# Kernel tuning notes

Measured on AMD Instinct MI355X. Metric: run time of the kernel, lower is better.

Reference implementation:

```python
import jax, jax.numpy as jnp
import numpy as np

B, Q, D = 8, 128, 2048
H, HD = 16, 128           # num_heads, head_dim (D == H*HD)
CACHE = 3968              # tokens already in KV cache; CACHE+Q == max_seq_len


def setup_inputs() -> dict:
    key = jax.random.key(0)
    ks = jax.random.split(key, 6)
    x = jax.random.normal(ks[0], (B, Q, D), dtype=jnp.float32)
    k_cache = jax.random.normal(ks[1], (B, H, CACHE, HD), dtype=jnp.float32)
    v_cache = jax.random.normal(ks[2], (B, H, CACHE, HD), dtype=jnp.float32)
    Wqkv = jax.random.normal(ks[3], (D, 3 * D), dtype=jnp.float32) * 0.02
    Wproj = jax.random.normal(ks[4], (D, D), dtype=jnp.float32) * 0.02
    bproj = jnp.zeros((D,), dtype=jnp.float32)
    return {"x": x, "k_cache": k_cache, "v_cache": v_cache,
            "Wqkv": Wqkv, "Wproj": Wproj, "bproj": bproj}


def reference(x, k_cache, v_cache, Wqkv, Wproj, bproj):
    # QKV projection (qkv_bias=False)
    qkv = x @ Wqkv                                   # [B, Q, 3D]
    qkv = qkv.reshape(B, Q, 3, H, HD)
    qkv = jnp.transpose(qkv, (2, 0, 3, 1, 4))        # [3, B, H, Q, HD]
    q, k_new, v_new = qkv[0], qkv[1], qkv[2]
    # KV-cache append (cache_pos + Q == max_seq_len, no roll)
    k_all = jnp.concatenate([k_cache, k_new], axis=2)  # [B, H, K, HD]
    v_all = jnp.concatenate([v_cache, v_new], axis=2)
    K = CACHE + Q
    scale = 1.0 / jnp.sqrt(jnp.float32(HD))
    scores = jnp.einsum('bhqd,bhkd->bhqk', q, k_all) * scale  # [B, H, Q, K]
    # Causal mask aligned to cache (bottom-right): query i sees keys j <= i + (K - Q)
    i = jnp.arange(Q)[:, None]
    j = jnp.arange(K)[None, :]
    mask = j > (i + (K - Q))
    scores = jnp.where(mask, jnp.float32(-jnp.inf), scores)
    attn = jax.nn.softmax(scores, axis=-1)
    out = jnp.einsum('bhqk,bhkd->bhqd', attn, v_all)   # [B, H, Q, HD]
    out = jnp.transpose(out, (0, 2, 1, 3)).reshape(B, Q, D)
    return out @ Wproj + bproj
```

## Files before the change

### kernel.cpp

```cpp
#include <hip/hip_runtime.h>

typedef unsigned int u32;
typedef unsigned short u16;
typedef short s16x8 __attribute__((ext_vector_type(8)));
typedef float f32x4 __attribute__((ext_vector_type(4)));

#define MFMA16(a,b,c) __builtin_amdgcn_mfma_f32_16x16x32_bf16((a),(b),(c),0,0,0)

#define Bb 8
#define Hh 16
#define Qq 128
#define HDd 128
#define Dd 2048
#define CACHE 3968
#define NSPLIT 8
#define SCALE 0.08838834764831845f
#define SM_OFF 8.0f

__device__ __forceinline__ u16 f2bf(float x){
  u32 u = __builtin_bit_cast(u32, x);
  u32 r = ((u >> 16) & 1u) + 0x7fffu;
  return (u16)((u + r) >> 16);
}
__device__ __forceinline__ float bf2f(u16 h){
  return __builtin_bit_cast(float, ((u32)h) << 16);
}
__device__ __forceinline__ u32 pk2(float a, float b){
  return (u32)f2bf(a) | ((u32)f2bf(b) << 16);
}
__device__ __forceinline__ float f4c(const float4& v, int j){
  return j==0 ? v.x : j==1 ? v.y : j==2 ? v.z : v.w;
}
__device__ __forceinline__ void gload_lds16(const void* g, void* l){
  __builtin_amdgcn_global_load_lds(
      (const __attribute__((address_space(1))) u32*)g,
      (__attribute__((address_space(3))) u32*)l, 16, 0, 0);
}
__device__ __forceinline__ void lgkm_barrier(){
  asm volatile("s_waitcnt lgkmcnt(0)" ::: "memory");
  __builtin_amdgcn_s_barrier();
}

__global__ void k_cvt(const float* __restrict__ s, u16* __restrict__ d, int n4){
  int i = blockIdx.x * 256 + threadIdx.x;
  if (i < n4){
    float4 v = *(const float4*)(s + (size_t)i * 4);
    *(uint2*)(d + (size_t)i * 4) = make_uint2(pk2(v.x, v.y), pk2(v.z, v.w));
  }
}

__global__ void k_tcvt(const float* __restrict__ s, u16* __restrict__ d, int R, int C){
  __shared__ float t[32][33];
  int tx = threadIdx.x & 31, ty = threadIdx.x >> 5;
  int c0 = blockIdx.x * 32, r0 = blockIdx.y * 32;
#pragma unroll
  for (int i = 0; i < 4; i++)
    t[ty + i*8][tx] = s[(size_t)(r0 + ty + i*8) * C + c0 + tx];
  __syncthreads();
#pragma unroll
  for (int i = 0; i < 4; i++)
    d[(size_t)(c0 + ty + i*8) * R + r0 + tx] = f2bf(t[tx][ty + i*8]);
}

template<int MODE>
__global__ __launch_bounds__(256)
void k_gemm(const u16* __restrict__ A, const u16* __restrict__ Bt, int K, int N,
            u16* __restrict__ oq, u16* __restrict__ ok, u16* __restrict__ ov,
            float* __restrict__ of, const float* __restrict__ bias)
{
  const int m0 = blockIdx.y * 128, n0 = blockIdx.x * 128;
  const int tid = threadIdx.x;
  const int w = tid >> 6, l = tid & 63;
  const int lg = l >> 4, lr = l & 15;
  const int wr = w >> 1, wc = w & 1;

  __shared__ u16 As[2][128 * 32];
  __shared__ u16 Bs[2][128 * 32];

  f32x4 acc[4][4];
#pragma unroll
  for (int i = 0; i < 4; i++)
#pragma unroll
    for (int j = 0; j < 4; j++) acc[i][j] = f32x4{0.f, 0.f, 0.f, 0.f};

  const int nt = K >> 5;

  auto stage = [&](int buf, int t){
    const int k0 = t << 5;
#pragma unroll
    for (int i = 0; i < 2; i++){
      int flat = i * 256 + tid;
      int row = flat >> 2, kq = flat & 3;
      const u16* ga = A + (size_t)(m0 + row) * K + k0 + kq * 8;
      gload_lds16(ga, (char*)&As[buf][0] + (size_t)(i*256 + w*64) * 16);
      const u16* gb = Bt + (size_t)(n0 + row) * K + k0 + kq * 8;
      gload_lds16(gb, (char*)&Bs[buf][0] + (size_t)(i*256 + w*64) * 16);
    }
  };

  stage(0, 0);
  asm volatile("s_waitcnt vmcnt(0)" ::: "memory");
  __syncthreads();

  for (int t = 0; t < nt; ++t){
    const int buf = t & 1;
    if (t + 1 < nt) stage(buf ^ 1, t + 1);
    s16x8 af[4], bfr[4];
#pragma unroll
    for (int i = 0; i < 4; i++){
      int row = wr*64 + i*16 + lr;
      af[i] = *(const s16x8*)&As[buf][row*32 + lg*8];
    }
#pragma unroll
    for (int j = 0; j < 4; j++){
      int col = wc*64 + j*16 + lr;
      bfr[j] = *(const s16x8*)&Bs[buf][col*32 + lg*8];
    }
#pragma unroll
    for (int i = 0; i < 4; i++)
#pragma unroll
      for (int j = 0; j < 4; j++)
        acc[i][j] = MFMA16(af[i], bfr[j], acc[i][j]);
    asm volatile("s_waitcnt vmcnt(0)" ::: "memory");
    __syncthreads();
  }

#pragma unroll
  for (int i = 0; i < 4; i++){
#pragma unroll
    for (int j = 0; j < 4; j++){
#pragma unroll
      for (int r = 0; r < 4; r++){
        int m = m0 + wr*64 + i*16 + lg*4 + r;
        int n = n0 + wc*64 + j*16 + lr;
        float v = acc[i][j][r];
        if (MODE == 0){
          int which = n >> 11;
          int h = (n >> 7) & 15, hd = n & 127;
          int b = m >> 7, qi = m & 127;
          size_t idx = (((size_t)(b * Hh + h)) * Qq + qi) * HDd + hd;
          if (which == 0)      oq[idx] = f2bf(v * SCALE);
          else if (which == 1) ok[idx] = f2bf(v);
          else                 ov[idx] = f2bf(v);
        } else {
          of[(size_t)m * N + n] = v + bias[n];
        }
      }
    }
  }
}

__global__ __launch_bounds__(512, 2)
void k_attn(const float* __restrict__ kc, const float* __restrict__ vc,
            const u16* __restrict__ qw, const u16* __restrict__ knw,
            const u16* __restrict__ vnw, float* __restrict__ opart,
            float2* __restrict__ ml)
{
  const int tid = threadIdx.x;
  const int w = tid >> 6, l = tid & 63;
  const int lg = l >> 4, lr = l & 15;

  __shared__ __align__(16) u16 Ks[2][64 * 136];
  __shared__ u32 Vts[128 * 32];

  const int rv = tid & 15, c4v = tid >> 4;

#pragma unroll 1
  for (int rep = 0; rep < 2; ++rep){
    const int vb = blockIdx.x * 2 + rep;
    const int bh = vb >> 3;
    const int sg = vb & 7;

    s16x8 qf[4];
    {
      const u16* qp = qw + (((size_t)bh * Qq + w*16 + lr) * HDd);
#pragma unroll
      for (int kk = 0; kk < 4; kk++) qf[kk] = *(const s16x8*)(qp + kk*32 + lg*8);
    }

    f32x4 acc[8];
#pragma unroll
    for (int i = 0; i < 8; i++) acc[i] = f32x4{0.f, 0.f, 0.f, 0.f};
    float lpart = 0.f;

    const float* kbase = kc + (size_t)bh * CACHE * HDd;
    const float* vbase = vc + (size_t)bh * CACHE * HDd;
    const u16* knb = knw + (size_t)bh * Qq * HDd;
    const u16* vnb = vnw + (size_t)bh * Qq * HDd;

    float4 kreg[4], vreg[4];

    auto loadc = [&](int c){
      if (c < 62){
#pragma unroll
        for (int i = 0; i < 4; i++){
          int flat = tid + i*512;
          int row = flat >> 5, c4 = flat & 31;
          kreg[i] = *(const float4*)(kbase + ((size_t)(c*64 + row)) * HDd + c4*4);
        }
#pragma unroll
        for (int a = 0; a < 4; a++)
          vreg[a] = *(const float4*)(vbase + ((size_t)(c*64 + rv + a*16)) * HDd + c4v*4);
      } else {
#pragma unroll
        for (int i = 0; i < 4; i++){
          int flat = tid + i*512;
          int row = flat >> 5, c4 = flat & 31;
          ushort4 u = *(const ushort4*)(knb + ((size_t)(c*64 + row - CACHE)) * HDd + c4*4);
          kreg[i] = make_float4(bf2f(u.x), bf2f(u.y), bf2f(u.z), bf2f(u.w));
        }
#pragma unroll
        for (int a = 0; a < 4; a++){
          ushort4 u = *(const ushort4*)(vnb + ((size_t)(c*64 + rv + a*16 - CACHE)) * HDd + c4v*4);
          vreg[a] = make_float4(bf2f(u.x), bf2f(u.y), bf2f(u.z), bf2f(u.w));
        }
      }
    };

    auto writeK = [&](int buf){
#pragma unroll
      for (int i = 0; i < 4; i++){
        int flat = tid + i*512;
        int row = flat >> 5, c4 = flat & 31;
        *(uint2*)&Ks[buf][row*136 + c4*4] =
            make_uint2(pk2(kreg[i].x, kreg[i].y), pk2(kreg[i].z, kreg[i].w));
      }
    };
    auto writeV = [&](){
#pragma unroll
      for (int j = 0; j < 4; j++){
        int col = c4v*4 + j;
        int x2 = (col & 7) << 2;
        Vts[col*32 + (rv ^ x2)]        = pk2(f4c(vreg[0], j), f4c(vreg[1], j));
        Vts[col*32 + ((rv + 16) ^ x2)] = pk2(f4c(vreg[2], j), f4c(vreg[3], j));
      }
    };

    int cur = 0;
    loadc(sg * 8);
    writeK(0);
    writeV();
    __syncthreads();

    for (int cl = 0; cl < 8; ++cl){
      const int c = sg * 8 + cl;
      if (cl + 1 < 8) loadc(c + 1);

      f32x4 s[4];
      __builtin_amdgcn_s_setprio(1);
#pragma unroll
      for (int t = 0; t < 4; t++){
        s[t] = f32x4{0.f, 0.f, 0.f, 0.f};
        const u16* kp = &Ks[cur][(t*16 + lr) * 136];
#pragma unroll
        for (int kk = 0; kk < 4; kk++){
          s16x8 kf = *(const s16x8*)(kp + kk*32 + lg*8);
          s[t] = MFMA16(kf, qf[kk], s[t]);
        }
      }
      __builtin_amdgcn_s_setprio(0);

      if (c >= 62){
        int jn = c*64 - CACHE;
        int qi = w*16 + lr;
#pragma unroll
        for (int t = 0; t < 4; t++)
#pragma unroll
          for (int r = 0; r < 4; r++){
            int kn = jn + t*16 + lg*4 + r;
            if (kn > qi) s[t][r] = -__builtin_inff();
          }
      }

      float ps = 0.f;
#pragma unroll
      for (int t = 0; t < 4; t++)
#pragma unroll
        for (int r = 0; r < 4; r++){
          float p = __expf(s[t][r] - SM_OFF);
          s[t][r] = p;
          ps += p;
        }
      lpart += ps;

      s16x8 pf[2];
      {
        union { uint4 u; s16x8 v; } c0, c1;
        c0.u = make_uint4(pk2(s[0][0], s[1][0]), pk2(s[0][1], s[1][1]),
                          pk2(s[0][2], s[1][2]), pk2(s[0][3], s[1][3]));
        c1.u = make_uint4(pk2(s[2][0], s[3][0]), pk2(s[2][1], s[3][1]),
                          pk2(s[2][2], s[3][2]), pk2(s[2][3], s[3][3]));
        pf[0] = c0.v;
        pf[1] = c1.v;
      }

      if (cl + 1 < 8) writeK(cur ^ 1);

      lgkm_barrier();

      __builtin_amdgcn_s_setprio(1);
#pragma unroll
      for (int t = 0; t < 8; t++){
        int col = t*16 + lr;
        const u32* vp = &Vts[col * 32];
#pragma unroll
        for (int kk = 0; kk < 2; kk++){
          s16x8 vf = *(const s16x8*)(vp + ((16*kk + 4*lg) ^ ((col & 7) << 2)));
          acc[t] = MFMA16(vf, pf[kk], acc[t]);
        }
      }
      __builtin_amdgcn_s_setprio(0);

      lgkm_barrier();

      if (cl + 1 < 8) writeV();

      cur ^= 1;
    }

    float lsum = lpart;
    lsum += __shfl_xor(lsum, 16);
    lsum += __shfl_xor(lsum, 32);

    float* pbase = opart + (size_t)vb * (Qq * HDd);
    float* Lt = (float*)Ks;
#pragma unroll 1
    for (int half = 0; half < 2; half++){
      if ((w >> 2) == half){
        int ql = (w & 3) * 16 + lr;
#pragma unroll
        for (int t = 0; t < 8; t++)
#pragma unroll
          for (int r = 0; r < 4; r++)
            Lt[ql * 132 + t*16 + lg*4 + r] = acc[t][r];
      }
      __syncthreads();
      {
        int c32 = tid & 31;
#pragma unroll
        for (int j = 0; j < 4; j++){
          int ql = (tid >> 5) + j * 16;
          float4 v = *(const float4*)&Lt[ql * 132 + c32 * 4];
          *(float4*)&pbase[(size_t)(half * 64 + ql) * HDd + c32 * 4] = v;
        }
      }
      __syncthreads();
    }
    if (lg == 0)
      ml[(size_t)vb * Qq + w*16 + lr] = make_float2(SM_OFF, lsum);
    __syncthreads();
  }
}

__global__ __launch_bounds__(256)
void k_comb(const float* __restrict__ opart, const float2* __restrict__ ml,
            u16* __restrict__ ao)
{
  const int bh = blockIdx.x >> 2;
  const int q0 = (blockIdx.x & 3) * 32;
  const int tid = threadIdx.x;

  __shared__ float wgt[32][NSPLIT];
  __shared__ float Ls[32];

  {
    int row = tid >> 3, s = tid & 7;
    float2 v = ml[((size_t)(bh * NSPLIT + s)) * Qq + q0 + row];
    float m = v.x;
    m = fmaxf(m, __shfl_xor(m, 1));
    m = fmaxf(m, __shfl_xor(m, 2));
    m = fmaxf(m, __shfl_xor(m, 4));
    float e = __expf(v.x - m);
    float el = e * v.y;
    el += __shfl_xor(el, 1);
    el += __shfl_xor(el, 2);
    el += __shfl_xor(el, 4);
    wgt[row][s] = e;
    if (s == 0) Ls[row] = el;
  }
  __syncthreads();

  const int cp = tid & 63;
  const int r4 = tid >> 6;
  const int b = bh >> 4, h = bh & 15;
#pragma unroll
  for (int rr = 0; rr < 8; rr++){
    int row = r4 + rr*4;
    float2 a = make_float2(0.f, 0.f);
    const float* pb = opart + ((size_t)(bh * NSPLIT)) * (Qq * HDd)
                            + (size_t)(q0 + row) * HDd + cp*2;
#pragma unroll
    for (int s = 0; s < NSPLIT; s++){
      float2 p = *(const float2*)(pb + (size_t)s * (Qq * HDd));
      float wv = wgt[row][s];
      a.x += wv * p.x;
      a.y += wv * p.y;
    }
    float inv = 1.0f / Ls[row];
    u16* dst = ao + ((size_t)b * Qq + q0 + row) * Dd + h * HDd + cp*2;
    *(u32*)dst = pk2(a.x * inv, a.y * inv);
  }
}

extern "C" void kernel_launch(void* const* d_in, const int* in_sizes, int n_in,
                              void* d_out, int out_size, void* d_ws, size_t ws_size,
                              hipStream_t stream)
{
  const float* x     = (const float*)d_in[0];
  const float* kc    = (const float*)d_in[1];
  const float* vc    = (const float*)d_in[2];
  const float* wqkv  = (const float*)d_in[3];
  const float* wproj = (const float*)d_in[4];
  const float* bproj = (const float*)d_in[5];
  float* out = (float*)d_out;

  char* ws = (char*)d_ws;
  u16* xb  = (u16*)(ws);
  u16* wtq = (u16*)(ws + ((size_t)4  << 20));
  u16* wtp = (u16*)(ws + ((size_t)28 << 20));
  u16* qw  = (u16*)(ws + ((size_t)36 << 20));
  u16* knw = (u16*)(ws + ((size_t)40 << 20));
  u16* vnw = (u16*)(ws + ((size_t)44 << 20));
  u16* aow = (u16*)(ws + ((size_t)48 << 20));
  float* opart = (float*)(ws + ((size_t)52 << 20));
  float2* mlw  = (float2*)(ws + ((size_t)116 << 20));

  k_cvt<<<2048, 256, 0, stream>>>(x, xb, (1024 * 2048) / 4);
  k_tcvt<<<dim3(192, 64), 256, 0, stream>>>(wqkv, wtq, 2048, 6144);
  k_tcvt<<<dim3(64, 64), 256, 0, stream>>>(wproj, wtp, 2048, 2048);
  k_gemm<0><<<dim3(48, 8), 256, 0, stream>>>(xb, wtq, 2048, 6144,
                                             qw, knw, vnw, nullptr, nullptr);
  k_attn<<<512, 512, 0, stream>>>(kc, vc, qw, knw, vnw, opart, mlw);
  k_comb<<<Bb * Hh * 4, 256, 0, stream>>>(opart, mlw, aow);
  k_gemm<1><<<dim3(16, 8), 256, 0, stream>>>(aow, wtp, 2048, 2048,
                                             nullptr, nullptr, nullptr, out, bproj);
}
```

Measured before the change: 281.9 us.

## Double-buffer V tile in LDS and use hardware bf16 pack conversion

Turns the transposed V tile in shared memory into a double buffer, so the next chunk's V is written into the spare buffer while the current one feeds the PV MFMAs. This removes one of the two barriers per chunk iteration. The software round-to-nearest bf16 packing is also replaced with the v_cvt_pk_bf16_f32 instruction. The cost is 16KB more LDS per block, which may limit the two-blocks-per-CU occupancy, and the hardware conversion may round special values differently.

After: 276.7 us. No clear change (-1.9%).

```diff
diff --git a/kernel.cpp b/kernel.cpp
--- a/kernel.cpp
+++ b/kernel.cpp
@@ -27,6 +27,11 @@
 }
 __device__ __forceinline__ u32 pk2(float a, float b){
   return (u32)f2bf(a) | ((u32)f2bf(b) << 16);
+}
+__device__ __forceinline__ u32 cvtpk(float a, float b){
+  u32 r;
+  asm("v_cvt_pk_bf16_f32 %0, %1, %2" : "=v"(r) : "v"(a), "v"(b));
+  return r;
 }
 __device__ __forceinline__ float f4c(const float4& v, int j){
   return j==0 ? v.x : j==1 ? v.y : j==2 ? v.z : v.w;
@@ -161,7 +166,7 @@
   const int lg = l >> 4, lr = l & 15;
 
   __shared__ __align__(16) u16 Ks[2][64 * 136];
-  __shared__ u32 Vts[128 * 32];
+  __shared__ u32 Vts[2][128 * 32];
 
   const int rv = tid & 15, c4v = tid >> 4;
 
@@ -223,23 +228,23 @@
         int flat = tid + i*512;
         int row = flat >> 5, c4 = flat & 31;
         *(uint2*)&Ks[buf][row*136 + c4*4] =
-            make_uint2(pk2(kreg[i].x, kreg[i].y), pk2(kreg[i].z, kreg[i].w));
+            make_uint2(cvtpk(kreg[i].x, kreg[i].y), cvtpk(kreg[i].z, kreg[i].w));
       }
     };
-    auto writeV = [&](){
+    auto writeV = [&](int buf){
 #pragma unroll
       for (int j = 0; j < 4; j++){
         int col = c4v*4 + j;
         int x2 = (col & 7) << 2;
-        Vts[col*32 + (rv ^ x2)]        = pk2(f4c(vreg[0], j), f4c(vreg[1], j));
-        Vts[col*32 + ((rv + 16) ^ x2)] = pk2(f4c(vreg[2], j), f4c(vreg[3], j));
+        Vts[buf][col*32 + (rv ^ x2)]        = cvtpk(f4c(vreg[0], j), f4c(vreg[1], j));
+        Vts[buf][col*32 + ((rv + 16) ^ x2)] = cvtpk(f4c(vreg[2], j), f4c(vreg[3], j));
       }
     };
 
     int cur = 0;
     loadc(sg * 8);
     writeK(0);
-    writeV();
+    writeV(0);
     __syncthreads();
 
     for (int cl = 0; cl < 8; ++cl){
@@ -286,23 +291,21 @@
       s16x8 pf[2];
       {
         union { uint4 u; s16x8 v; } c0, c1;
-        c0.u = make_uint4(pk2(s[0][0], s[1][0]), pk2(s[0][1], s[1][1]),
-                          pk2(s[0][2], s[1][2]), pk2(s[0][3], s[1][3]));
-        c1.u = make_uint4(pk2(s[2][0], s[3][0]), pk2(s[2][1], s[3][1]),
-                          pk2(s[2][2], s[3][2]), pk2(s[2][3], s[3][3]));
+        c0.u = make_uint4(cvtpk(s[0][0], s[1][0]), cvtpk(s[0][1], s[1][1]),
+                          cvtpk(s[0][2], s[1][2]), cvtpk(s[0][3], s[1][3]));
+        c1.u = make_uint4(cvtpk(s[2][0], s[3][0]), cvtpk(s[2][1], s[3][1]),
+                          cvtpk(s[2][2], s[3][2]), cvtpk(s[2][3], s[3][3]));
         pf[0] = c0.v;
         pf[1] = c1.v;
       }
 
       if (cl + 1 < 8) writeK(cur ^ 1);
 
-      lgkm_barrier();
-
       __builtin_amdgcn_s_setprio(1);
 #pragma unroll
       for (int t = 0; t < 8; t++){
         int col = t*16 + lr;
-        const u32* vp = &Vts[col * 32];
+        const u32* vp = &Vts[cur][col * 32];
 #pragma unroll
         for (int kk = 0; kk < 2; kk++){
           s16x8 vf = *(const s16x8*)(vp + ((16*kk + 4*lg) ^ ((col & 7) << 2)));
@@ -311,10 +314,9 @@
       }
       __builtin_amdgcn_s_setprio(0);
 
+      if (cl + 1 < 8) writeV(cur ^ 1);
+
       lgkm_barrier();
-
-      if (cl + 1 < 8) writeV();
-
       cur ^= 1;
     }
 
```
